# Performance work log

Hardware: AMD Instinct MI355X
Metric: run time of the kernel (lower is better)

## Reference

```python
import jax, jax.numpy as jnp
import numpy as np

ROUTINGS = 3
EPS = 1e-7  # tf.keras.backend.epsilon()


def _squash(s):
    # s: (B, num_caps, cap_dim)
    n = jnp.linalg.norm(s, axis=-1, keepdims=True)
    return (n ** 2 / (1.0 + n ** 2)) * s / (n + EPS)


def setup_inputs() -> dict:
    key = jax.random.key(0)
    k1, k2 = jax.random.split(key)
    B, N, D_IN, M, C = 64, 2048, 16, 32, 16
    inputs = jax.random.normal(k1, (B, N, D_IN), dtype=jnp.float32)
    # he_normal: std = sqrt(2 / fan_in), fan_in = D_IN for the (1, D_IN, M*C) kernel
    W = jax.random.normal(k2, (D_IN, M, C), dtype=jnp.float32) * np.float32(np.sqrt(2.0 / D_IN))
    return {"inputs": inputs, "W": W}


def reference(inputs, W):
    # prediction vectors u_hat: (B, N, num_caps, cap_dim)
    u_hat = jnp.einsum('bnd,dmc->bnmc', inputs, W)
    b = jnp.zeros(u_hat.shape[:3], dtype=u_hat.dtype)  # (B, N, num_caps)
    v = None
    for _ in range(ROUTINGS):  # fixed small routing count
        c = jax.nn.softmax(b, axis=1)                      # over input capsules
        s = jnp.einsum('bnm,bnmc->bmc', c, u_hat)          # weighted sum
        v = _squash(s)                                     # (B, num_caps, cap_dim)
        b = b + jnp.einsum('bmc,bnmc->bnm', v, u_hat)      # agreement update
    return v
```

## Files before the change

kernel.cpp:

```cpp
#include <hip/hip_runtime.h>
#include <math.h>


#define TPB 1024
#define LOG2E 1.44269504088896f

typedef __attribute__((ext_vector_type(8))) short short8;
typedef __attribute__((ext_vector_type(4))) short short4v;
typedef __attribute__((ext_vector_type(4))) float float4v;

#if defined(__has_builtin)
#if __has_builtin(__builtin_amdgcn_mfma_f32_16x16x16bf16_1k)
#define HAVE_MFMA16 1
#endif
#endif

#define DPP_ADDF(x, ctrl) \
    ((x) + __int_as_float(__builtin_amdgcn_update_dpp( \
        0, __float_as_int(x), (ctrl), 0xF, 0xF, true)))

static __device__ inline unsigned short f2bf(float x) {
    unsigned u = __float_as_uint(x);
    return (unsigned short)((u + 0x7FFFu + ((u >> 16) & 1u)) >> 16);
}
static __device__ inline unsigned pk2(float a, float b) {
    return (unsigned)f2bf(a) | ((unsigned)f2bf(b) << 16);
}

__global__ __launch_bounds__(TPB)
void capsule_routing_kernel(const float* __restrict__ in,
                            const float* __restrict__ W,
                            float* __restrict__ out)
{
    __shared__ unsigned short inT[16 * 2056];
    __shared__ float scratch[16][320];
    __shared__ unsigned short cumT[16 * 24];
    __shared__ float tbx[4][64];

    const int tid  = threadIdx.x;
    const int w    = tid >> 6;
    const int l    = tid & 63;
    const int ml   = l & 15;
    const int quad = l >> 4;
    const int b    = blockIdx.x & 63;
    const int m0g  = (blockIdx.x >> 6) << 4;

    const float4* gin4 = (const float4*)(in + ((size_t)b << 15));

    float4 ga0, ga1, ga2, ga3, gb0, gb1, gb2, gb3;
    {
        const int nb0 = (w << 7);
        ga0 = gin4[(nb0       + ml) * 4 + quad];
        gb0 = gin4[(nb0 + 16  + ml) * 4 + quad];
        ga1 = gin4[(nb0 + 32  + ml) * 4 + quad];
        gb1 = gin4[(nb0 + 48  + ml) * 4 + quad];
        ga2 = gin4[(nb0 + 64  + ml) * 4 + quad];
        gb2 = gin4[(nb0 + 80  + ml) * 4 + quad];
        ga3 = gin4[(nb0 + 96  + ml) * 4 + quad];
        gb3 = gin4[(nb0 + 112 + ml) * 4 + quad];
    }
    const int m  = tid >> 4;
    const int tc = tid & 15;
    const int wt = tid >> 6;
    const int mr = m & 3;
    float Wcol[16];
    float4 Wr0, Wr1, Wr2, Wr3;
    if (tid < 256) {
        const float* Wb = &W[((m0g + m) << 4) + tc];
        #pragma unroll
        for (int d = 0; d < 16; ++d)
            Wcol[d] = Wb[d << 9];
        const float4* Wrow = (const float4*)&W[(tc << 9) + ((m0g + m) << 4)];
        Wr0 = Wrow[0]; Wr1 = Wrow[1]; Wr2 = Wrow[2]; Wr3 = Wrow[3];
    }

#ifdef HAVE_MFMA16
    short4v a0h[4], a1h[4];
#else
    short8 a0h[4], a1h[4];
#endif
    short8 bih[4];
    {
        float cs0 = (ga0.x + gb0.x) + (ga1.x + gb1.x) + (ga2.x + gb2.x) + (ga3.x + gb3.x);
        float cs1 = (ga0.y + gb0.y) + (ga1.y + gb1.y) + (ga2.y + gb2.y) + (ga3.y + gb3.y);
        float cs2 = (ga0.z + gb0.z) + (ga1.z + gb1.z) + (ga2.z + gb2.z) + (ga3.z + gb3.z);
        float cs3 = (ga0.w + gb0.w) + (ga1.w + gb1.w) + (ga2.w + gb2.w) + (ga3.w + gb3.w);

        const float4 gaa[4] = {ga0, ga1, ga2, ga3};
        const float4 gbb[4] = {gb0, gb1, gb2, gb3};
        #pragma unroll
        for (int t = 0; t < 4; ++t) {
            const int nb = (w << 7) + (t << 5);
            const float4 ga = gaa[t];
            const float4 gb = gbb[t];
            const unsigned short a0 = f2bf(ga.x), a1 = f2bf(ga.y),
                                 a2 = f2bf(ga.z), a3 = f2bf(ga.w);
            const unsigned short b0 = f2bf(gb.x), b1 = f2bf(gb.y),
                                 b2 = f2bf(gb.z), b3 = f2bf(gb.w);
#ifdef HAVE_MFMA16
            short4v av; av[0]=(short)a0; av[1]=(short)a1; av[2]=(short)a2; av[3]=(short)a3;
            short4v bv; bv[0]=(short)b0; bv[1]=(short)b1; bv[2]=(short)b2; bv[3]=(short)b3;
            a0h[t] = av; a1h[t] = bv;
#else
            short8 av = {0,0,0,0,0,0,0,0}, bv = {0,0,0,0,0,0,0,0};
            a0h[t] = av; a1h[t] = bv;
#endif
            const int dbase = quad * 4;
            inT[(dbase + 0) * 2056 + nb + ml]      = a0;
            inT[(dbase + 1) * 2056 + nb + ml]      = a1;
            inT[(dbase + 2) * 2056 + nb + ml]      = a2;
            inT[(dbase + 3) * 2056 + nb + ml]      = a3;
            inT[(dbase + 0) * 2056 + nb + 16 + ml] = b0;
            inT[(dbase + 1) * 2056 + nb + 16 + ml] = b1;
            inT[(dbase + 2) * 2056 + nb + 16 + ml] = b2;
            inT[(dbase + 3) * 2056 + nb + 16 + ml] = b3;
            bih[t] = *(const short8*)&inT[ml * 2056 + nb + quad * 8];
        }
        cs0 = DPP_ADDF(cs0, 0xB1); cs0 = DPP_ADDF(cs0, 0x4E);
        cs1 = DPP_ADDF(cs1, 0xB1); cs1 = DPP_ADDF(cs1, 0x4E);
        cs2 = DPP_ADDF(cs2, 0xB1); cs2 = DPP_ADDF(cs2, 0x4E);
        cs3 = DPP_ADDF(cs3, 0xB1); cs3 = DPP_ADDF(cs3, 0x4E);
        cs0 = DPP_ADDF(cs0, 0x104); cs0 = DPP_ADDF(cs0, 0x108);
        cs1 = DPP_ADDF(cs1, 0x104); cs1 = DPP_ADDF(cs1, 0x108);
        cs2 = DPP_ADDF(cs2, 0x104); cs2 = DPP_ADDF(cs2, 0x108);
        cs3 = DPP_ADDF(cs3, 0x104); cs3 = DPP_ADDF(cs3, 0x108);
        if ((l & 15) == 0) {
            float4 v4; v4.x = cs0; v4.y = cs1; v4.z = cs2; v4.w = cs3;
            *(float4*)&scratch[w][quad * 4] = v4;
        }
    }

    const int srcAB = ml + ((quad == 0) ? 16 : (quad == 1) ? 32 : 0);
    const int srcCD = ml + ((quad == 1) ? 48 : (quad == 3) ? 32 : 16);
    const bool selAB = (quad == 1) || (quad == 2);
    const bool selC  = (quad == 3);

    float cwv = 0.f;

    for (int pass = 0; pass < 3; ++pass) {
        if (pass) {
#ifdef HAVE_MFMA16
            const short4v bc = *(const short4v*)&cumT[ml * 24 + quad * 4];
#else
            short8 bc = {0,0,0,0,0,0,0,0};
            if (quad < 2)
                bc = *(const short8*)&cumT[ml * 24 + quad * 8];
#endif
            float4v xc = {0.f, 0.f, 0.f, 0.f};
            float Sp = 0.f;

            #pragma unroll
            for (int t = 0; t < 4; ++t) {
                const float4v z = {0.f, 0.f, 0.f, 0.f};
#ifdef HAVE_MFMA16
                float4v c0 = __builtin_amdgcn_mfma_f32_16x16x16bf16_1k(a0h[t], bc, z, 0, 0, 0);
                float4v c1 = __builtin_amdgcn_mfma_f32_16x16x16bf16_1k(a1h[t], bc, z, 0, 0, 0);
#else
                float4v c0 = __builtin_amdgcn_mfma_f32_16x16x32_bf16(a0h[t], bc, z, 0, 0, 0);
                float4v c1 = __builtin_amdgcn_mfma_f32_16x16x32_bf16(a1h[t], bc, z, 0, 0, 0);
#endif
                float e00 = exp2f(c0[0]), e01 = exp2f(c0[1]),
                      e02 = exp2f(c0[2]), e03 = exp2f(c0[3]);
                float e10 = exp2f(c1[0]), e11 = exp2f(c1[1]),
                      e12 = exp2f(c1[2]), e13 = exp2f(c1[3]);
                Sp += (e00 + e01) + (e02 + e03) + (e10 + e11) + (e12 + e13);
                const unsigned d00 = pk2(e00, e01), d01 = pk2(e02, e03);
                const unsigned d10 = pk2(e10, e11), d11 = pk2(e12, e13);
                const unsigned RA = (unsigned)__shfl((int)(selAB ? d00 : d10), srcAB);
                const unsigned RB = (unsigned)__shfl((int)(selAB ? d01 : d11), srcAB);
                const unsigned RC = (unsigned)__shfl((int)(selC  ? d00 : d10), srcCD);
                const unsigned RD = (unsigned)__shfl((int)(selC  ? d01 : d11), srcCD);
                union { unsigned u[4]; short8 s; } ua;
                ua.u[0] = (quad == 0) ? d00 : (selC ? RC : RA);
                ua.u[1] = (quad == 0) ? d01 : (selC ? RD : RB);
                ua.u[2] = (quad == 0) ? RA  : (selC ? d10 : RC);
                ua.u[3] = (quad == 0) ? RB  : (selC ? d11 : RD);
                xc = __builtin_amdgcn_mfma_f32_16x16x32_bf16(ua.s, bih[t], xc, 0, 0, 0);
            }
            Sp += __shfl_xor(Sp, 16);
            Sp += __shfl_xor(Sp, 32);
            #pragma unroll
            for (int r = 0; r < 4; ++r)
                scratch[w][(quad * 4 + r) * 17 + ml] = xc[r];
            if (l < 16) scratch[w][272 + l] = Sp;
        }
        __syncthreads();

        if (tid < 256) {
            float Stot, xtot = 0.f;
            if (pass == 0) {
                Stot = 2048.f;
                #pragma unroll
                for (int w2 = 0; w2 < 16; ++w2)
                    xtot += scratch[w2][tc];
            } else {
                Stot = 0.f;
                #pragma unroll
                for (int w2 = 0; w2 < 16; ++w2) {
                    Stot += scratch[w2][272 + m];
                    xtot += scratch[w2][m * 17 + tc];
                }
            }
            tbx[wt][mr * 16 + tc] = xtot;
            const float4 x0 = *(const float4*)&tbx[wt][mr * 16 + 0];
            const float4 x1 = *(const float4*)&tbx[wt][mr * 16 + 4];
            const float4 x2 = *(const float4*)&tbx[wt][mr * 16 + 8];
            const float4 x3 = *(const float4*)&tbx[wt][mr * 16 + 12];
            float s = x0.x * Wcol[0]  + x0.y * Wcol[1]
                    + x0.z * Wcol[2]  + x0.w * Wcol[3]
                    + x1.x * Wcol[4]  + x1.y * Wcol[5]
                    + x1.z * Wcol[6]  + x1.w * Wcol[7]
                    + x2.x * Wcol[8]  + x2.y * Wcol[9]
                    + x2.z * Wcol[10] + x2.w * Wcol[11]
                    + x3.x * Wcol[12] + x3.y * Wcol[13]
                    + x3.z * Wcol[14] + x3.w * Wcol[15];
            s /= Stot;
            tbx[wt][mr * 16 + tc] = s;
            const float4 s0 = *(const float4*)&tbx[wt][mr * 16 + 0];
            const float4 s1 = *(const float4*)&tbx[wt][mr * 16 + 4];
            const float4 s2 = *(const float4*)&tbx[wt][mr * 16 + 8];
            const float4 s3 = *(const float4*)&tbx[wt][mr * 16 + 12];
            const float n2 = s0.x*s0.x + s0.y*s0.y + s0.z*s0.z + s0.w*s0.w
                           + s1.x*s1.x + s1.y*s1.y + s1.z*s1.z + s1.w*s1.w
                           + s2.x*s2.x + s2.y*s2.y + s2.z*s2.z + s2.w*s2.w
                           + s3.x*s3.x + s3.y*s3.y + s3.z*s3.z + s3.w*s3.w;
            const float fac = (n2 / (1.f + n2)) / (sqrtf(n2) + 1e-7f);
            if (pass < 2) {
                const float wdot =
                      Wr0.x*s0.x + Wr0.y*s0.y + Wr0.z*s0.z + Wr0.w*s0.w
                    + Wr1.x*s1.x + Wr1.y*s1.y + Wr1.z*s1.z + Wr1.w*s1.w
                    + Wr2.x*s2.x + Wr2.y*s2.y + Wr2.z*s2.z + Wr2.w*s2.w
                    + Wr3.x*s3.x + Wr3.y*s3.y + Wr3.z*s3.z + Wr3.w*s3.w;
                cwv += fac * wdot;
                cumT[m * 24 + tc] = f2bf(cwv * LOG2E);
            } else {
                out[((size_t)b << 9) + ((m0g + m) << 4) + tc] = s * fac;
            }
        }
        if (pass < 2) __syncthreads();
    }
}

extern "C" void kernel_launch(void* const* d_in, const int* in_sizes, int n_in,
                              void* d_out, int out_size, void* d_ws, size_t ws_size,
                              hipStream_t stream) {
    (void)in_sizes; (void)n_in; (void)d_ws; (void)ws_size; (void)out_size;
    const float* in = (const float*)d_in[0];
    const float* W  = (const float*)d_in[1];
    float* out = (float*)d_out;
    hipLaunchKernelGGL(capsule_routing_kernel, dim3(128), dim3(TPB), 0, stream,
                       in, W, out);
}
```

Measured before the change: 68.02 us.

## Process all 32 output capsules per block, halving grid to one block per batch

Each block now handles all 32 output capsules for one batch element instead of 16, so the grid drops from 128 to 64 blocks. The input load, transposition and column-sum work per batch is done once instead of twice, and the MFMA routing loop computes two capsule groups per wave. The cost is that only 64 of the GPU's compute units get work, and each block has more serial work and higher register and shared-memory use.

```diff
diff --git a/kernel.cpp b/kernel.cpp
--- a/kernel.cpp
+++ b/kernel.cpp
@@ -33,17 +33,16 @@
                             float* __restrict__ out)
 {
     __shared__ unsigned short inT[16 * 2056];
-    __shared__ float scratch[16][320];
-    __shared__ unsigned short cumT[16 * 24];
-    __shared__ float tbx[4][64];
+    __shared__ float scratch[16][576];
+    __shared__ unsigned short cumT[32 * 24];
+    __shared__ float tbx[8][64];
 
     const int tid  = threadIdx.x;
     const int w    = tid >> 6;
     const int l    = tid & 63;
     const int ml   = l & 15;
     const int quad = l >> 4;
-    const int b    = blockIdx.x & 63;
-    const int m0g  = (blockIdx.x >> 6) << 4;
+    const int b    = blockIdx.x;
 
     const float4* gin4 = (const float4*)(in + ((size_t)b << 15));
 
@@ -65,12 +64,12 @@
     const int mr = m & 3;
     float Wcol[16];
     float4 Wr0, Wr1, Wr2, Wr3;
-    if (tid < 256) {
-        const float* Wb = &W[((m0g + m) << 4) + tc];
+    if (tid < 512) {
+        const float* Wb = &W[(m << 4) + tc];
         #pragma unroll
         for (int d = 0; d < 16; ++d)
             Wcol[d] = Wb[d << 9];
-        const float4* Wrow = (const float4*)&W[(tc << 9) + ((m0g + m) << 4)];
+        const float4* Wrow = (const float4*)&W[(tc << 9) + (m << 4)];
         Wr0 = Wrow[0]; Wr1 = Wrow[1]; Wr2 = Wrow[2]; Wr3 = Wrow[3];
     }
 
@@ -140,53 +139,89 @@
     for (int pass = 0; pass < 3; ++pass) {
         if (pass) {
 #ifdef HAVE_MFMA16
-            const short4v bc = *(const short4v*)&cumT[ml * 24 + quad * 4];
-#else
-            short8 bc = {0,0,0,0,0,0,0,0};
-            if (quad < 2)
-                bc = *(const short8*)&cumT[ml * 24 + quad * 8];
-#endif
-            float4v xc = {0.f, 0.f, 0.f, 0.f};
-            float Sp = 0.f;
+            const short4v bc0 = *(const short4v*)&cumT[ml * 24 + quad * 4];
+            const short4v bc1 = *(const short4v*)&cumT[(16 + ml) * 24 + quad * 4];
+#else
+            short8 bc0 = {0,0,0,0,0,0,0,0}, bc1 = {0,0,0,0,0,0,0,0};
+            if (quad < 2) {
+                bc0 = *(const short8*)&cumT[ml * 24 + quad * 8];
+                bc1 = *(const short8*)&cumT[(16 + ml) * 24 + quad * 8];
+            }
+#endif
+            float4v xc0 = {0.f, 0.f, 0.f, 0.f};
+            float4v xc1 = {0.f, 0.f, 0.f, 0.f};
+            float Sp0 = 0.f, Sp1 = 0.f;
 
             #pragma unroll
             for (int t = 0; t < 4; ++t) {
                 const float4v z = {0.f, 0.f, 0.f, 0.f};
 #ifdef HAVE_MFMA16
-                float4v c0 = __builtin_amdgcn_mfma_f32_16x16x16bf16_1k(a0h[t], bc, z, 0, 0, 0);
-                float4v c1 = __builtin_amdgcn_mfma_f32_16x16x16bf16_1k(a1h[t], bc, z, 0, 0, 0);
-#else
-                float4v c0 = __builtin_amdgcn_mfma_f32_16x16x32_bf16(a0h[t], bc, z, 0, 0, 0);
-                float4v c1 = __builtin_amdgcn_mfma_f32_16x16x32_bf16(a1h[t], bc, z, 0, 0, 0);
-#endif
-                float e00 = exp2f(c0[0]), e01 = exp2f(c0[1]),
-                      e02 = exp2f(c0[2]), e03 = exp2f(c0[3]);
-                float e10 = exp2f(c1[0]), e11 = exp2f(c1[1]),
-                      e12 = exp2f(c1[2]), e13 = exp2f(c1[3]);
-                Sp += (e00 + e01) + (e02 + e03) + (e10 + e11) + (e12 + e13);
-                const unsigned d00 = pk2(e00, e01), d01 = pk2(e02, e03);
-                const unsigned d10 = pk2(e10, e11), d11 = pk2(e12, e13);
-                const unsigned RA = (unsigned)__shfl((int)(selAB ? d00 : d10), srcAB);
-                const unsigned RB = (unsigned)__shfl((int)(selAB ? d01 : d11), srcAB);
-                const unsigned RC = (unsigned)__shfl((int)(selC  ? d00 : d10), srcCD);
-                const unsigned RD = (unsigned)__shfl((int)(selC  ? d01 : d11), srcCD);
-                union { unsigned u[4]; short8 s; } ua;
-                ua.u[0] = (quad == 0) ? d00 : (selC ? RC : RA);
-                ua.u[1] = (quad == 0) ? d01 : (selC ? RD : RB);
-                ua.u[2] = (quad == 0) ? RA  : (selC ? d10 : RC);
-                ua.u[3] = (quad == 0) ? RB  : (selC ? d11 : RD);
-                xc = __builtin_amdgcn_mfma_f32_16x16x32_bf16(ua.s, bih[t], xc, 0, 0, 0);
-            }
-            Sp += __shfl_xor(Sp, 16);
-            Sp += __shfl_xor(Sp, 32);
+                float4v c0 = __builtin_amdgcn_mfma_f32_16x16x16bf16_1k(a0h[t], bc0, z, 0, 0, 0);
+                float4v c1 = __builtin_amdgcn_mfma_f32_16x16x16bf16_1k(a1h[t], bc0, z, 0, 0, 0);
+                float4v d0 = __builtin_amdgcn_mfma_f32_16x16x16bf16_1k(a0h[t], bc1, z, 0, 0, 0);
+                float4v d1 = __builtin_amdgcn_mfma_f32_16x16x16bf16_1k(a1h[t], bc1, z, 0, 0, 0);
+#else
+                float4v c0 = __builtin_amdgcn_mfma_f32_16x16x32_bf16(a0h[t], bc0, z, 0, 0, 0);
+                float4v c1 = __builtin_amdgcn_mfma_f32_16x16x32_bf16(a1h[t], bc0, z, 0, 0, 0);
+                float4v d0 = __builtin_amdgcn_mfma_f32_16x16x32_bf16(a0h[t], bc1, z, 0, 0, 0);
+                float4v d1 = __builtin_amdgcn_mfma_f32_16x16x32_bf16(a1h[t], bc1, z, 0, 0, 0);
+#endif
+                {
+                    float e00 = exp2f(c0[0]), e01 = exp2f(c0[1]),
+                          e02 = exp2f(c0[2]), e03 = exp2f(c0[3]);
+                    float e10 = exp2f(c1[0]), e11 = exp2f(c1[1]),
+                          e12 = exp2f(c1[2]), e13 = exp2f(c1[3]);
+                    Sp0 += (e00 + e01) + (e02 + e03) + (e10 + e11) + (e12 + e13);
+                    const unsigned d00 = pk2(e00, e01), d01 = pk2(e02, e03);
+                    const unsigned d10 = pk2(e10, e11), d11 = pk2(e12, e13);
+                    const unsigned RA = (unsigned)__shfl((int)(selAB ? d00 : d10), srcAB);
+                    const unsigned RB = (unsigned)__shfl((int)(selAB ? d01 : d11), srcAB);
+                    const unsigned RC = (unsigned)__shfl((int)(selC  ? d00 : d10), srcCD);
+                    const unsigned RD = (unsigned)__shfl((int)(selC  ? d01 : d11), srcCD);
+                    union { unsigned u[4]; short8 s; } ua;
+                    ua.u[0] = (quad == 0) ? d00 : (selC ? RC : RA);
+                    ua.u[1] = (quad == 0) ? d01 : (selC ? RD : RB);
+                    ua.u[2] = (quad == 0) ? RA  : (selC ? d10 : RC);
+                    ua.u[3] = (quad == 0) ? RB  : (selC ? d11 : RD);
+                    xc0 = __builtin_amdgcn_mfma_f32_16x16x32_bf16(ua.s, bih[t], xc0, 0, 0, 0);
+                }
+                {
+                    float e00 = exp2f(d0[0]), e01 = exp2f(d0[1]),
+                          e02 = exp2f(d0[2]), e03 = exp2f(d0[3]);
+                    float e10 = exp2f(d1[0]), e11 = exp2f(d1[1]),
+                          e12 = exp2f(d1[2]), e13 = exp2f(d1[3]);
+                    Sp1 += (e00 + e01) + (e02 + e03) + (e10 + e11) + (e12 + e13);
+                    const unsigned d00 = pk2(e00, e01), d01 = pk2(e02, e03);
+                    const unsigned d10 = pk2(e10, e11), d11 = pk2(e12, e13);
+                    const unsigned RA = (unsigned)__shfl((int)(selAB ? d00 : d10), srcAB);
+                    const unsigned RB = (unsigned)__shfl((int)(selAB ? d01 : d11), srcAB);
+                    const unsigned RC = (unsigned)__shfl((int)(selC  ? d00 : d10), srcCD);
+                    const unsigned RD = (unsigned)__shfl((int)(selC  ? d01 : d11), srcCD);
+                    union { unsigned u[4]; short8 s; } ua;
+                    ua.u[0] = (quad == 0) ? d00 : (selC ? RC : RA);
+                    ua.u[1] = (quad == 0) ? d01 : (selC ? RD : RB);
+                    ua.u[2] = (quad == 0) ? RA  : (selC ? d10 : RC);
+                    ua.u[3] = (quad == 0) ? RB  : (selC ? d11 : RD);
+                    xc1 = __builtin_amdgcn_mfma_f32_16x16x32_bf16(ua.s, bih[t], xc1, 0, 0, 0);
+                }
+            }
+            Sp0 += __shfl_xor(Sp0, 16);
+            Sp0 += __shfl_xor(Sp0, 32);
+            Sp1 += __shfl_xor(Sp1, 16);
+            Sp1 += __shfl_xor(Sp1, 32);
             #pragma unroll
-            for (int r = 0; r < 4; ++r)
-                scratch[w][(quad * 4 + r) * 17 + ml] = xc[r];
-            if (l < 16) scratch[w][272 + l] = Sp;
+            for (int r = 0; r < 4; ++r) {
+                scratch[w][(quad * 4 + r) * 17 + ml]        = xc0[r];
+                scratch[w][(16 + quad * 4 + r) * 17 + ml]   = xc1[r];
+            }
+            if (l < 16) {
+                scratch[w][544 + l]      = Sp0;
+                scratch[w][544 + 16 + l] = Sp1;
+            }
         }
         __syncthreads();
 
-        if (tid < 256) {
+        if (tid < 512) {
             float Stot, xtot = 0.f;
             if (pass == 0) {
                 Stot = 2048.f;
@@ -197,7 +232,7 @@
                 Stot = 0.f;
                 #pragma unroll
                 for (int w2 = 0; w2 < 16; ++w2) {
-                    Stot += scratch[w2][272 + m];
+                    Stot += scratch[w2][544 + m];
                     xtot += scratch[w2][m * 17 + tc];
                 }
             }
@@ -234,7 +269,7 @@
                 cwv += fac * wdot;
                 cumT[m * 24 + tc] = f2bf(cwv * LOG2E);
             } else {
-                out[((size_t)b << 9) + ((m0g + m) << 4) + tc] = s * fac;
+                out[((size_t)b << 9) + (m << 4) + tc] = s * fac;
             }
         }
         if (pass < 2) __syncthreads();
@@ -248,6 +283,6 @@
     const float* in = (const float*)d_in[0];
     const float* W  = (const float*)d_in[1];
     float* out = (float*)d_out;
-    hipLaunchKernelGGL(capsule_routing_kernel, dim3(128), dim3(TPB), 0, stream,
+    hipLaunchKernelGGL(capsule_routing_kernel, dim3(64), dim3(TPB), 0, stream,
                        in, W, out);
 }
```

New measurement: 74.80 us. 1.1x slower.
